# Kernel optimization log

Measured on AMD Instinct MI355X. Metric: run time of the kernel, lower is better.

## Reference

```python
import jax, jax.numpy as jnp
import numpy as np

BS, TS, NE, ED = 32, 64, 64, 128
AE = 256          # attn_embed_dim
NH = 4            # attn heads
HD = AE // NH     # head dim
RH = 256          # rnn_hidden_dim
NA = 8            # n_agents
NACT = 64         # n_actions
NEG = -1e10


def setup_inputs() -> dict:
    key = jax.random.key(0)
    ks = iter(jax.random.split(key, 64))
    def g(shape, s=0.05):
        return jax.random.normal(next(ks), shape, dtype=jnp.float32) * s
    inp = dict(
        entities=g((BS, TS, NE, ED), 1.0),
        obs_mask=jax.random.randint(next(ks), (BS, TS, NE, NE), 0, 2, dtype=jnp.int32),
        entity_mask=jax.random.randint(next(ks), (BS, TS, NE), 0, 2, dtype=jnp.int32),
        hidden_q=g((BS, NA, RH), 1.0),
        hidden_pi=g((BS, NA, RH), 1.0),
    )
    for p in ('q', 'p'):
        inp[f'{p}_fc1_w'] = g((AE, ED)); inp[f'{p}_fc1_b'] = g((AE,))
        inp[f'{p}_fc2_w'] = g((RH, AE)); inp[f'{p}_fc2_b'] = g((RH,))
        inp[f'{p}_gru_wih'] = g((3 * RH, RH)); inp[f'{p}_gru_whh'] = g((3 * RH, RH))
        inp[f'{p}_gru_bih'] = g((3 * RH,)); inp[f'{p}_gru_bhh'] = g((3 * RH,))
        inp[f'{p}_fcq_w'] = g((NACT, RH)); inp[f'{p}_fcq_b'] = g((NACT,))
        inp[f'{p}_fcpi_w'] = g((NACT, RH)); inp[f'{p}_fcpi_b'] = g((NACT,))
    inp['q_attn_in_w'] = g((3 * AE, AE))
    inp['q_attn_out_w'] = g((AE, AE)); inp['q_attn_out_b'] = g((AE,))
    return inp


def _attention(x1, pre_mask, in_w, out_w, out_b):
    # x1: [B, NE, AE]; pre_mask: [B, NA, NE] (1 = masked)
    qkv = x1 @ in_w.T                                   # [B, NE, 3*AE]
    q, k, v = jnp.split(qkv, 3, axis=-1)
    q = q[:, :NA].reshape(-1, NA, NH, HD).transpose(0, 2, 1, 3)   # [B,H,NA,HD]
    k = k.reshape(-1, NE, NH, HD).transpose(0, 2, 1, 3)           # [B,H,NE,HD]
    v = v.reshape(-1, NE, NH, HD).transpose(0, 2, 1, 3)
    logits = jnp.einsum('bhqd,bhkd->bhqk', q, k) / jnp.sqrt(jnp.float32(HD))
    m = (pre_mask[:, None, :, :] != 0)                  # [B,1,NA,NE]
    dead = jnp.all(m, axis=-1, keepdims=True)           # fully-masked rows -> NaN fix
    logits = jnp.where(m, -jnp.inf, logits)
    logits = jnp.where(dead, 0.0, logits)
    w = jax.nn.softmax(logits, axis=-1)
    w = jnp.where(dead, 0.0, w)                         # torch: masked_fill(NaN, 0)
    out = jnp.einsum('bhqk,bhkd->bhqd', w, v)
    out = out.transpose(0, 2, 1, 3).reshape(-1, NA, AE)
    return out @ out_w.T + out_b


def _gru_scan(x3, h0, wih, whh, bih, bhh):
    # x3: [BS, TS, NA, RH]; h0: [BS*NA, RH]
    xt = x3.transpose(1, 0, 2, 3).reshape(TS, BS * NA, RH)
    def step(h, x):
        gi = x @ wih.T + bih
        gh = h @ whh.T + bhh
        ir, iz, inn = jnp.split(gi, 3, axis=-1)
        hr, hz, hn = jnp.split(gh, 3, axis=-1)
        r = jax.nn.sigmoid(ir + hr)
        z = jax.nn.sigmoid(iz + hz)
        n = jnp.tanh(inn + r * hn)
        h_new = (1.0 - z) * n + z * h
        return h_new, h_new
    _, hs = jax.lax.scan(step, h0, xt)
    return hs.reshape(TS, BS, NA, RH).transpose(1, 0, 2, 3)       # [BS,TS,NA,RH]


def _module(entities, obs_mask, entity_mask, hidden, use_attn,
            fc1_w, fc1_b, fc2_w, fc2_b, gru_wih, gru_whh, gru_bih, gru_bhh,
            fcq_w, fcq_b, fcpi_w, fcpi_b, attn=None):
    B = BS * TS
    e = entities.reshape(B, NE, ED)
    om = obs_mask.reshape(B, NE, NE)
    em = entity_mask.reshape(B, NE)
    agent_mask = em[:, :NA]                              # [B, NA]
    x1 = jax.nn.relu(e @ fc1_w.T + fc1_b)                # [B, NE, AE]
    if use_attn:
        in_w, out_w, out_b = attn
        x2 = _attention(x1, om[:, :NA], in_w, out_w, out_b)
        x2 = jnp.where(agent_mask[:, :, None] != 0, 0.0, x2)   # post_mask
    else:
        x2 = x1[:, :NA]
    x3 = jax.nn.relu(x2 @ fc2_w.T + fc2_b).reshape(BS, TS, NA, RH)
    hs = _gru_scan(x3, hidden.reshape(-1, RH), gru_wih, gru_whh, gru_bih, gru_bhh)
    oq = hs @ fcq_w.T + fcq_b
    opi = hs @ fcpi_w.T + fcpi_b
    am = (agent_mask.reshape(BS, TS, NA, 1) != 0)
    oq = jnp.where(am, 0.0, oq)
    opi = jnp.where(am, NEG, opi)
    return oq, opi, hs


def reference(entities, obs_mask, entity_mask, hidden_q, hidden_pi,
              q_fc1_w, q_fc1_b, q_attn_in_w, q_attn_out_w, q_attn_out_b,
              q_fc2_w, q_fc2_b, q_gru_wih, q_gru_whh, q_gru_bih, q_gru_bhh,
              q_fcq_w, q_fcq_b, q_fcpi_w, q_fcpi_b,
              p_fc1_w, p_fc1_b, p_fc2_w, p_fc2_b,
              p_gru_wih, p_gru_whh, p_gru_bih, p_gru_bhh,
              p_fcq_w, p_fcq_b, p_fcpi_w, p_fcpi_b):
    q, pi, h_q = _module(entities, obs_mask, entity_mask, hidden_q, True,
                         q_fc1_w, q_fc1_b, q_fc2_w, q_fc2_b,
                         q_gru_wih, q_gru_whh, q_gru_bih, q_gru_bhh,
                         q_fcq_w, q_fcq_b, q_fcpi_w, q_fcpi_b,
                         attn=(q_attn_in_w, q_attn_out_w, q_attn_out_b))
    _, pi_avg, h_pi = _module(entities, obs_mask, entity_mask, hidden_pi, False,
                              p_fc1_w, p_fc1_b, p_fc2_w, p_fc2_b,
                              p_gru_wih, p_gru_whh, p_gru_bih, p_gru_bhh,
                              p_fcq_w, p_fcq_b, p_fcpi_w, p_fcpi_b)
    return (q, pi, pi_avg, h_q, h_pi)
```

## Files before the change

### kernel.cpp

```cpp
#include <hip/hip_runtime.h>

typedef unsigned short ushort_t;
typedef __attribute__((ext_vector_type(4))) float f32x4;
typedef __attribute__((ext_vector_type(8))) short s16x8;
typedef __attribute__((ext_vector_type(4))) short s16x4;

#define MFMA16(a, b, c) __builtin_amdgcn_mfma_f32_16x16x32_bf16((a), (b), (c), 0, 0, 0)

__device__ __forceinline__ float us2f(unsigned short u) {
  union { unsigned int i; float f; } v; v.i = ((unsigned int)u) << 16; return v.f;
}
__device__ __forceinline__ unsigned short f2us(float f) {
  union { float f; unsigned int i; } v; v.f = f;
  unsigned int x = v.i;
  return (unsigned short)((x + 0x7FFFu + ((x >> 16) & 1u)) >> 16);
}
__device__ __forceinline__ s16x8 ld8f(const float* p) {
  f32x4 a = *reinterpret_cast<const f32x4*>(p);
  f32x4 b = *reinterpret_cast<const f32x4*>(p + 4);
  s16x8 r;
  r[0] = (short)f2us(a[0]); r[1] = (short)f2us(a[1]);
  r[2] = (short)f2us(a[2]); r[3] = (short)f2us(a[3]);
  r[4] = (short)f2us(b[0]); r[5] = (short)f2us(b[1]);
  r[6] = (short)f2us(b[2]); r[7] = (short)f2us(b[3]);
  return r;
}
__device__ __forceinline__ float sigm(float x) { return 1.0f / (1.0f + __expf(-x)); }
__device__ __forceinline__ float tanh_f(float x) {
  float e = __expf(-2.0f * fabsf(x));
  float t = (1.0f - e) / (1.0f + e);
  return x < 0.0f ? -t : t;
}

__global__ __launch_bounds__(256) void conv_k(
    const float* __restrict__ s0, const float* __restrict__ s1,
    const float* __restrict__ s2, const float* __restrict__ s3,
    ushort_t* __restrict__ d) {
  int i = blockIdx.x * 256 + threadIdx.x;
  if (i >= 155648) return;
  long e = (long)i * 4;
  const float* s; long off;
  if (e < 196608) { s = s0; off = e; }
  else if (e < 393216) { s = s1; off = e - 196608; }
  else if (e < 425984) { s = s2; off = e - 393216; }
  else { s = s3; off = e - 425984; }
  f32x4 v = *reinterpret_cast<const f32x4*>(s + off);
  s16x4 r;
  r[0] = (short)f2us(v[0]); r[1] = (short)f2us(v[1]);
  r[2] = (short)f2us(v[2]); r[3] = (short)f2us(v[3]);
  *reinterpret_cast<s16x4*>(d + e) = r;
}

template <int BN, int EPI, int ROWSEL, int RELU, int AF32, int WF32, int OF32,
          int QKV, int HB>
__global__ __launch_bounds__(256) void gemm_k(
    const void* __restrict__ A_, const void* __restrict__ W_,
    const float* __restrict__ bias, const int* __restrict__ em,
    void* __restrict__ out_, ushort_t* __restrict__ qout, long row0,
    int M, int N, int K,
    const void* __restrict__ A2_, const void* __restrict__ W2_,
    const float* __restrict__ bias2, void* __restrict__ out2_) {
  constexpr int NF = BN / 32;
  if (A2_ != nullptr && blockIdx.z != 0) {
    A_ = A2_; W_ = W2_; bias = bias2; out_ = out2_;
  }
  const float* Af = (const float*)A_;
  const ushort_t* Ab = (const ushort_t*)A_;
  const float* Wf = (const float*)W_;
  const ushort_t* Wb = (const ushort_t*)W_;
  float* outf = (float*)out_;
  ushort_t* outb = (ushort_t*)out_;
  __shared__ ushort_t As[128 * 40];
  __shared__ ushort_t Ws[BN * 40];
  const int tid = threadIdx.x;
  const int lane = tid & 63;
  const int wid = tid >> 6;
  const int wm = wid & 1, wn = wid >> 1;
  const int m0 = blockIdx.x * 128;
  const int n0 = blockIdx.y * BN;
  const int fr = lane & 15;
  const int kb = (lane >> 4) * 8;
  const int rb = (lane >> 4) * 4;

  f32x4 acc[4][NF];
#pragma unroll
  for (int i = 0; i < 4; i++)
#pragma unroll
    for (int j = 0; j < NF; j++) acc[i][j] = (f32x4){0.f, 0.f, 0.f, 0.f};

  for (int k0 = 0; k0 < K; k0 += 32) {
    __syncthreads();
    for (int c = tid; c < 512; c += 256) {
      int row = c >> 2, kc = (c & 3) * 8;
      int gr = m0 + row;
      long ar = ROWSEL ? ((long)(gr >> 3) * 64 + (gr & 7)) : (long)gr;
      s16x8 vv;
      if (AF32) vv = ld8f(&Af[ar * (long)K + k0 + kc]);
      else vv = *reinterpret_cast<const s16x8*>(&Ab[ar * (long)K + k0 + kc]);
      *reinterpret_cast<s16x8*>(&As[row * 40 + kc]) = vv;
    }
    for (int c = tid; c < BN * 4; c += 256) {
      int row = c >> 2, kc = (c & 3) * 8;
      s16x8 wv;
      if (WF32) wv = ld8f(&Wf[(long)(n0 + row) * K + k0 + kc]);
      else wv = *reinterpret_cast<const s16x8*>(&Wb[(long)(n0 + row) * K + k0 + kc]);
      *reinterpret_cast<s16x8*>(&Ws[row * 40 + kc]) = wv;
    }
    __syncthreads();
    s16x8 af[4], wf[NF];
#pragma unroll
    for (int mi = 0; mi < 4; mi++)
      af[mi] = *reinterpret_cast<const s16x8*>(&As[(wm * 64 + mi * 16 + fr) * 40 + kb]);
#pragma unroll
    for (int ni = 0; ni < NF; ni++)
      wf[ni] = *reinterpret_cast<const s16x8*>(&Ws[(wn * (BN / 2) + ni * 16 + fr) * 40 + kb]);
#pragma unroll
    for (int mi = 0; mi < 4; mi++)
#pragma unroll
      for (int ni = 0; ni < NF; ni++) acc[mi][ni] = MFMA16(af[mi], wf[ni], acc[mi][ni]);
  }

#pragma unroll
  for (int ni = 0; ni < NF; ni++) {
    int col = n0 + wn * (BN / 2) + ni * 16 + fr;
    float bv = HB ? bias[col] : 0.0f;
#pragma unroll
    for (int mi = 0; mi < 4; mi++) {
#pragma unroll
      for (int rr = 0; rr < 4; rr++) {
        int row = m0 + wm * 64 + mi * 16 + rb + rr;
        float v = acc[mi][ni][rr] + bv;
        if (RELU) v = fmaxf(v, 0.0f);
        if (EPI == 2 || EPI == 3) {
          if (em[(long)(row >> 3) * 64 + (row & 7)] != 0) v = (EPI == 2) ? 0.0f : -1.0e10f;
        }
        if (QKV) {
          long grow = row0 + row;
          int e = (int)(grow & 63);
          if (col < 256) {
            if (e < 8) qout[((grow >> 6) * 8 + e) * 256 + col] = f2us(v * 0.125f);
          } else {
            outb[(long)row * 512 + (col - 256)] = f2us(v);
          }
        } else if (OF32) {
          outf[(long)row * N + col] = v;
        } else {
          outb[(long)row * N + col] = f2us(v);
        }
      }
    }
  }
}

__global__ __launch_bounds__(512) void attn2_k(
    const ushort_t* __restrict__ kv, const ushort_t* __restrict__ qbuf,
    const int* __restrict__ obs, ushort_t* __restrict__ attn_out, int b0) {
  __shared__ ushort_t qs[16 * 264];
  __shared__ ushort_t ks[64 * 264];
  __shared__ ushort_t vs[64 * 264];
  __shared__ float lg[32 * 66];
  __shared__ int oms[512];

  const int b_loc = blockIdx.x;
  const long b = b0 + b_loc;
  const int tid = threadIdx.x;
  const int lane = tid & 63;
  const int w = tid >> 6;
  const int fr = lane & 15, kb = (lane >> 4) * 8, rb = (lane >> 4) * 4;

  oms[tid] = obs[b * 4096 + tid];
  {
    int row = tid >> 5, cc = (tid & 31) * 8;
    if (tid < 256) {
      *reinterpret_cast<s16x8*>(&qs[row * 264 + cc]) =
          *reinterpret_cast<const s16x8*>(&qbuf[(b * 8 + row) * 256 + cc]);
    } else {
      *reinterpret_cast<s16x8*>(&qs[row * 264 + cc]) = (s16x8){0,0,0,0,0,0,0,0};
    }
  }
  for (int i = 0; i < 4; i++) {
    int e = i * 16 + (tid >> 5);
    int cc = (tid & 31) * 8;
    const ushort_t* src = &kv[((long)(b_loc * 64 + e)) * 512];
    *reinterpret_cast<s16x8*>(&ks[e * 264 + cc]) =
        *reinterpret_cast<const s16x8*>(&src[cc]);
    *reinterpret_cast<s16x8*>(&vs[e * 264 + cc]) =
        *reinterpret_cast<const s16x8*>(&src[256 + cc]);
  }
  __syncthreads();

  {
    const int h = w >> 1, np = w & 1;
    f32x4 lacc[2];
    lacc[0] = (f32x4){0.f, 0.f, 0.f, 0.f};
    lacc[1] = (f32x4){0.f, 0.f, 0.f, 0.f};
#pragma unroll
    for (int k0 = 0; k0 < 64; k0 += 32) {
      s16x8 af = *reinterpret_cast<const s16x8*>(&qs[fr * 264 + h * 64 + k0 + kb]);
#pragma unroll
      for (int j = 0; j < 2; j++) {
        int e0 = (np * 2 + j) * 16;
        s16x8 bf = *reinterpret_cast<const s16x8*>(&ks[(e0 + fr) * 264 + h * 64 + k0 + kb]);
        lacc[j] = MFMA16(af, bf, lacc[j]);
      }
    }
#pragma unroll
    for (int j = 0; j < 2; j++) {
      int e = (np * 2 + j) * 16 + fr;
#pragma unroll
      for (int rr = 0; rr < 4; rr++) {
        int a = rb + rr;
        if (a < 8)
          lg[(a * 4 + h) * 66 + e] = (oms[a * 64 + e] != 0) ? -1.0e30f : lacc[j][rr];
      }
    }
  }
  __syncthreads();

  {
    int ri = tid >> 4, sub = tid & 15;
    float v4[4];
#pragma unroll
    for (int j = 0; j < 4; j++) v4[j] = lg[ri * 66 + sub * 4 + j];
    float m = fmaxf(fmaxf(v4[0], v4[1]), fmaxf(v4[2], v4[3]));
#pragma unroll
    for (int d = 1; d < 16; d <<= 1) m = fmaxf(m, __shfl_xor(m, d));
    bool dead = (m < -5.0e29f);
    float s = 0.0f;
#pragma unroll
    for (int j = 0; j < 4; j++) { v4[j] = __expf(v4[j] - m); s += v4[j]; }
#pragma unroll
    for (int d = 1; d < 16; d <<= 1) s += __shfl_xor(s, d);
    float inv = dead ? 0.0f : (1.0f / s);
#pragma unroll
    for (int j = 0; j < 4; j++) lg[ri * 66 + sub * 4 + j] = v4[j] * inv;
  }
  __syncthreads();

  {
    int a = tid >> 6, d0 = (tid & 63) * 4, h = d0 >> 6;
    const float* wrow = &lg[(a * 4 + h) * 66];
    float facc[4] = {0.f, 0.f, 0.f, 0.f};
    for (int e = 0; e < 64; e++) {
      float wv = wrow[e];
      s16x4 vv = *reinterpret_cast<const s16x4*>(&vs[e * 264 + d0]);
#pragma unroll
      for (int j = 0; j < 4; j++) facc[j] += wv * us2f((unsigned short)vv[j]);
    }
    s16x4 r;
#pragma unroll
    for (int j = 0; j < 4; j++) r[j] = (short)f2us(facc[j]);
    *reinterpret_cast<s16x4*>(&attn_out[(b * 8 + a) * 256 + d0]) = r;
  }
}

__global__ __launch_bounds__(1024, 4) void gru4_k(
    const ushort_t* __restrict__ gi_q, const ushort_t* __restrict__ gi_p,
    const ushort_t* __restrict__ whhb_q, const ushort_t* __restrict__ whhb_p,
    const float* __restrict__ bhh_q, const float* __restrict__ bhh_p,
    const float* __restrict__ h0_q, const float* __restrict__ h0_p,
    float* __restrict__ hs_q, float* __restrict__ hs_p) {
  __shared__ ushort_t nw[256 * 256];
  __shared__ ushort_t hls[2][16 * 264];
  const int bid = blockIdx.x;
  const int mdl = bid >> 4, cg = bid & 15;
  const ushort_t* gi = mdl ? gi_p : gi_q;
  const ushort_t* whh = mdl ? whhb_p : whhb_q;
  const float* bhh = mdl ? bhh_p : bhh_q;
  const float* h0 = mdl ? h0_p : h0_q;
  float* hs = mdl ? hs_p : hs_q;

  const int tid = threadIdx.x;
  const int lane = tid & 63, w = tid >> 6;
  const int fr = lane & 15, kb = (lane >> 4) * 8, rb = (lane >> 4) * 4;
  const int col = w * 16 + fr;

  s16x8 wrz[2][8];
#pragma unroll
  for (int g = 0; g < 2; g++)
#pragma unroll
    for (int ks = 0; ks < 8; ks++)
      wrz[g][ks] = *reinterpret_cast<const s16x8*>(
          &whh[(g * 256 + col) * 256 + ks * 32 + kb]);

  char* nwb = (char*)nw;
  for (int c = tid; c < 8192; c += 1024) {
    int row = c >> 5, kc = (c & 31) * 8;
    *reinterpret_cast<s16x8*>(nwb + row * 512 + ((kc * 2) ^ ((row & 7) << 4))) =
        *reinterpret_cast<const s16x8*>(&whh[(512 + row) * 256 + kc]);
  }

  int nwaddr[8];
#pragma unroll
  for (int ks = 0; ks < 8; ks++)
    nwaddr[ks] = col * 512 + (((ks * 32 + kb) * 2) ^ ((col & 7) << 4));

  float h[4], bh[3];
#pragma unroll
  for (int rr = 0; rr < 4; rr++) h[rr] = h0[(cg * 16 + rb + rr) * 256 + col];
#pragma unroll
  for (int g = 0; g < 3; g++) bh[g] = bhh[g * 256 + col];

  const int chain0 = cg * 16 + rb;
  const long r0 = (long)(chain0 >> 3) * 512 + (chain0 & 7);
  const ushort_t* gp0 = gi + r0 * 768 + col;
  float* hp0 = hs + r0 * 256 + col;

#define GRU_STEP(BUF)                                                          \
  {                                                                            \
    float gv[3][4];                                                            \
    _Pragma("unroll") for (int rr = 0; rr < 4; rr++) {                         \
      gv[0][rr] = us2f(gp0[rr * 768]);                                         \
      gv[1][rr] = us2f(gp0[rr * 768 + 256]);                                   \
      gv[2][rr] = us2f(gp0[rr * 768 + 512]);                                   \
    }                                                                          \
    gp0 += 6144;                                                               \
    _Pragma("unroll") for (int rr = 0; rr < 4; rr++)                           \
        hls[BUF][(rb + rr) * 264 + col] = f2us(h[rr]);                         \
    __syncthreads();                                                           \
    f32x4 acc[3];                                                              \
    _Pragma("unroll") for (int i = 0; i < 3; i++)                              \
        acc[i] = (f32x4){0.f, 0.f, 0.f, 0.f};                                  \
    _Pragma("unroll") for (int ks = 0; ks < 8; ks++) {                         \
      s16x8 a = *reinterpret_cast<const s16x8*>(                               \
          &hls[BUF][fr * 264 + ks * 32 + kb]);                                 \
      acc[0] = MFMA16(a, wrz[0][ks], acc[0]);                                  \
      acc[1] = MFMA16(a, wrz[1][ks], acc[1]);                                  \
      s16x8 bn = *reinterpret_cast<const s16x8*>(nwb + nwaddr[ks]);            \
      acc[2] = MFMA16(a, bn, acc[2]);                                          \
    }                                                                          \
    _Pragma("unroll") for (int rr = 0; rr < 4; rr++) {                         \
      float r_ = sigm(gv[0][rr] + acc[0][rr] + bh[0]);                         \
      float z_ = sigm(gv[1][rr] + acc[1][rr] + bh[1]);                         \
      float n_ = tanh_f(gv[2][rr] + r_ * (acc[2][rr] + bh[2]));                \
      float hn = (1.0f - z_) * n_ + z_ * h[rr];                                \
      h[rr] = hn;                                                              \
      hp0[rr * 256] = hn;                                                      \
    }                                                                          \
    hp0 += 2048;                                                               \
  }

  for (int t2 = 0; t2 < 32; t2++) {
    GRU_STEP(0)
    GRU_STEP(1)
  }
#undef GRU_STEP
}

extern "C" void kernel_launch(void* const* d_in, const int* in_sizes, int n_in,
                              void* d_out, int out_size, void* d_ws, size_t ws_size,
                              hipStream_t stream) {
  (void)in_sizes; (void)n_in; (void)out_size; (void)ws_size;

  const float* entities = (const float*)d_in[0];
  const int* obs = (const int*)d_in[1];
  const int* em = (const int*)d_in[2];
  const float* hidq = (const float*)d_in[3];
  const float* hidp = (const float*)d_in[4];
  const float* q_fc1_w = (const float*)d_in[5];
  const float* q_fc1_b = (const float*)d_in[6];
  const float* q_fc2_w = (const float*)d_in[7];
  const float* q_fc2_b = (const float*)d_in[8];
  const float* q_wih = (const float*)d_in[9];
  const float* q_whh = (const float*)d_in[10];
  const float* q_bih = (const float*)d_in[11];
  const float* q_bhh = (const float*)d_in[12];
  const float* q_fcq_w = (const float*)d_in[13];
  const float* q_fcq_b = (const float*)d_in[14];
  const float* q_fcpi_w = (const float*)d_in[15];
  const float* q_fcpi_b = (const float*)d_in[16];
  const float* p_fc1_w = (const float*)d_in[17];
  const float* p_fc1_b = (const float*)d_in[18];
  const float* p_fc2_w = (const float*)d_in[19];
  const float* p_fc2_b = (const float*)d_in[20];
  const float* p_wih = (const float*)d_in[21];
  const float* p_whh = (const float*)d_in[22];
  const float* p_bih = (const float*)d_in[23];
  const float* p_bhh = (const float*)d_in[24];
  const float* p_fcpi_w = (const float*)d_in[27];
  const float* p_fcpi_b = (const float*)d_in[28];
  const float* inw = (const float*)d_in[29];
  const float* outw = (const float*)d_in[30];
  const float* outb = (const float*)d_in[31];

  ushort_t* ws = (ushort_t*)d_ws;
  ushort_t* qbuf = ws;
  ushort_t* attn = ws + 4194304l;
  ushort_t* x1c  = ws + 8388608l;
  ushort_t* kvc  = ws + 16777216l;
  ushort_t* wcv  = ws + 33554432l;
  ushort_t* wbq = wcv;
  ushort_t* wbp = wcv + 196608l;
  ushort_t* wf1 = wcv + 393216l;
  ushort_t* win = wcv + 425984l;
  ushort_t* x2b = ws + 35651584l;
  ushort_t* x3q = ws + 39845888l;
  ushort_t* x1p = ws + 44040192l;
  ushort_t* x3p = ws + 48234496l;
  ushort_t* giq = ws + 52428800l;
  ushort_t* gip = ws + 65011712l;

  float* out = (float*)d_out;
  float* o_q = out;
  float* o_pi = out + 1048576l;
  float* o_piA = out + 2097152l;
  float* o_hq = out + 3145728l;
  float* o_hp = out + 7340032l;

  const int nc = 4, CB = 512;
  const long MR = (long)CB * 64;
  const void* NUL = nullptr;

  conv_k<<<608, 256, 0, stream>>>(q_whh, p_whh, q_fc1_w, inw, wcv);

  for (int c = 0; c < nc; c++) {
    gemm_k<128, 0, 0, 1, 1, 0, 0, 0, 1><<<dim3(256, 2), 256, 0, stream>>>(
        entities + (long)c * MR * 128, wf1, q_fc1_b, em, x1c, nullptr, 0,
        (int)MR, 256, 128, NUL, NUL, nullptr, nullptr);
    gemm_k<128, 0, 0, 0, 0, 0, 0, 1, 0><<<dim3(256, 6), 256, 0, stream>>>(
        x1c, win, nullptr, em, kvc, qbuf, (long)c * MR, (int)MR, 768, 256,
        NUL, NUL, nullptr, nullptr);
    attn2_k<<<CB, 512, 0, stream>>>(kvc, qbuf, obs, attn, c * CB);
  }
  gemm_k<128, 2, 0, 0, 0, 1, 0, 0, 1><<<dim3(128, 2), 256, 0, stream>>>(
      attn, outw, outb, em, x2b, nullptr, 0, 16384, 256, 256,
      NUL, NUL, nullptr, nullptr);
  gemm_k<128, 0, 1, 1, 1, 1, 0, 0, 1><<<dim3(128, 2), 256, 0, stream>>>(
      entities, p_fc1_w, p_fc1_b, em, x1p, nullptr, 0, 16384, 256, 128,
      NUL, NUL, nullptr, nullptr);
  gemm_k<128, 0, 0, 1, 0, 1, 0, 0, 1><<<dim3(128, 2, 2), 256, 0, stream>>>(
      x2b, q_fc2_w, q_fc2_b, em, x3q, nullptr, 0, 16384, 256, 256,
      x1p, p_fc2_w, p_fc2_b, x3p);
  gemm_k<128, 0, 0, 0, 0, 1, 0, 0, 1><<<dim3(128, 6, 2), 256, 0, stream>>>(
      x3q, q_wih, q_bih, em, giq, nullptr, 0, 16384, 768, 256,
      x3p, p_wih, p_bih, gip);
  gru4_k<<<32, 1024, 0, stream>>>(giq, gip, wbq, wbp, q_bhh, p_bhh, hidq, hidp,
                                  o_hq, o_hp);
  gemm_k<64, 2, 0, 0, 1, 1, 1, 0, 1><<<dim3(128, 1), 256, 0, stream>>>(
      o_hq, q_fcq_w, q_fcq_b, em, o_q, nullptr, 0, 16384, 64, 256,
      NUL, NUL, nullptr, nullptr);
  gemm_k<64, 3, 0, 0, 1, 1, 1, 0, 1><<<dim3(128, 1, 2), 256, 0, stream>>>(
      o_hq, q_fcpi_w, q_fcpi_b, em, o_pi, nullptr, 0, 16384, 64, 256,
      o_hp, p_fcpi_w, p_fcpi_b, o_piA);
}
```

Measured before the change: 612.2 us.

## Batch fc1 GEMM into one launch, enlarge attention chunks, speed up GRU step

The fc1 projection now runs once over all entities instead of once per chunk, and the QKV and attention loop uses two chunks of 1024 instead of four of 512, so there are fewer, larger launches. The workspace layout is reshuffled so giq and gip alias the x1 buffer, which is dead by the time they are written. The GRU step uses packed bf16 conversion, folds the bias into the accumulator init, raises wave priority around the MFMA loop, and switches to rcp-based sigmoid and tanh. The fast activations change numerics slightly, and the aliased buffers depend on the order in which they are written and read.

```diff
diff --git a/kernel.cpp b/kernel.cpp
--- a/kernel.cpp
+++ b/kernel.cpp
@@ -30,6 +30,14 @@
   float e = __expf(-2.0f * fabsf(x));
   float t = (1.0f - e) / (1.0f + e);
   return x < 0.0f ? -t : t;
+}
+__device__ __forceinline__ float fast_sigm(float x) {
+  return __builtin_amdgcn_rcpf(1.0f + __expf(-x));
+}
+__device__ __forceinline__ float fast_tanh(float y) {
+  float yc = fminf(fmaxf(y, -15.0f), 15.0f);
+  float e2 = __expf(2.0f * yc);
+  return (e2 - 1.0f) * __builtin_amdgcn_rcpf(e2 + 1.0f);
 }
 
 __global__ __launch_bounds__(256) void conv_k(
@@ -254,7 +262,7 @@
   }
 }
 
-__global__ __launch_bounds__(1024, 4) void gru4_k(
+__global__ __launch_bounds__(1024, 4) void gru5_k(
     const ushort_t* __restrict__ gi_q, const ushort_t* __restrict__ gi_p,
     const ushort_t* __restrict__ whhb_q, const ushort_t* __restrict__ whhb_p,
     const float* __restrict__ bhh_q, const float* __restrict__ bhh_p,
@@ -305,8 +313,10 @@
   const long r0 = (long)(chain0 >> 3) * 512 + (chain0 & 7);
   const ushort_t* gp0 = gi + r0 * 768 + col;
   float* hp0 = hs + r0 * 256 + col;
-
-#define GRU_STEP(BUF)                                                          \
+  ushort_t* hrow0 = &hls[0][rb * 264 + col];
+  ushort_t* hrow1 = &hls[1][rb * 264 + col];
+
+#define GRU_STEP(HROW, BUF)                                                    \
   {                                                                            \
     float gv[3][4];                                                            \
     _Pragma("unroll") for (int rr = 0; rr < 4; rr++) {                         \
@@ -315,12 +325,18 @@
       gv[2][rr] = us2f(gp0[rr * 768 + 512]);                                   \
     }                                                                          \
     gp0 += 6144;                                                               \
-    _Pragma("unroll") for (int rr = 0; rr < 4; rr++)                           \
-        hls[BUF][(rb + rr) * 264 + col] = f2us(h[rr]);                         \
+    unsigned int pk01, pk23;                                                   \
+    asm("v_cvt_pk_bf16_f32 %0, %1, %2" : "=v"(pk01) : "v"(h[0]), "v"(h[1]));   \
+    asm("v_cvt_pk_bf16_f32 %0, %1, %2" : "=v"(pk23) : "v"(h[2]), "v"(h[3]));   \
+    HROW[0] = (ushort_t)(pk01 & 0xffffu);                                      \
+    HROW[264] = (ushort_t)(pk01 >> 16);                                        \
+    HROW[528] = (ushort_t)(pk23 & 0xffffu);                                    \
+    HROW[792] = (ushort_t)(pk23 >> 16);                                        \
     __syncthreads();                                                           \
     f32x4 acc[3];                                                              \
     _Pragma("unroll") for (int i = 0; i < 3; i++)                              \
-        acc[i] = (f32x4){0.f, 0.f, 0.f, 0.f};                                  \
+        acc[i] = (f32x4){bh[i], bh[i], bh[i], bh[i]};                          \
+    __builtin_amdgcn_s_setprio(1);                                             \
     _Pragma("unroll") for (int ks = 0; ks < 8; ks++) {                         \
       s16x8 a = *reinterpret_cast<const s16x8*>(                               \
           &hls[BUF][fr * 264 + ks * 32 + kb]);                                 \
@@ -329,11 +345,12 @@
       s16x8 bn = *reinterpret_cast<const s16x8*>(nwb + nwaddr[ks]);            \
       acc[2] = MFMA16(a, bn, acc[2]);                                          \
     }                                                                          \
+    __builtin_amdgcn_s_setprio(0);                                             \
     _Pragma("unroll") for (int rr = 0; rr < 4; rr++) {                         \
-      float r_ = sigm(gv[0][rr] + acc[0][rr] + bh[0]);                         \
-      float z_ = sigm(gv[1][rr] + acc[1][rr] + bh[1]);                         \
-      float n_ = tanh_f(gv[2][rr] + r_ * (acc[2][rr] + bh[2]));                \
-      float hn = (1.0f - z_) * n_ + z_ * h[rr];                                \
+      float r_ = fast_sigm(gv[0][rr] + acc[0][rr]);                            \
+      float z_ = fast_sigm(gv[1][rr] + acc[1][rr]);                            \
+      float n_ = fast_tanh(gv[2][rr] + r_ * acc[2][rr]);                       \
+      float hn = n_ + z_ * (h[rr] - n_);                                       \
       h[rr] = hn;                                                              \
       hp0[rr * 256] = hn;                                                      \
     }                                                                          \
@@ -341,8 +358,8 @@
   }
 
   for (int t2 = 0; t2 < 32; t2++) {
-    GRU_STEP(0)
-    GRU_STEP(1)
+    GRU_STEP(hrow0, 0)
+    GRU_STEP(hrow1, 1)
   }
 #undef GRU_STEP
 }
@@ -384,21 +401,21 @@
   const float* outb = (const float*)d_in[31];
 
   ushort_t* ws = (ushort_t*)d_ws;
-  ushort_t* qbuf = ws;
-  ushort_t* attn = ws + 4194304l;
-  ushort_t* x1c  = ws + 8388608l;
-  ushort_t* kvc  = ws + 16777216l;
-  ushort_t* wcv  = ws + 33554432l;
+  ushort_t* qbuf  = ws;
+  ushort_t* attn  = ws + 4194304l;
+  ushort_t* x1all = ws + 8388608l;
+  ushort_t* giq   = ws + 8388608l;
+  ushort_t* gip   = ws + 20971520l;
+  ushort_t* kvc   = ws + 41943040l;
+  ushort_t* wcv   = ws + 75497472l;
   ushort_t* wbq = wcv;
   ushort_t* wbp = wcv + 196608l;
   ushort_t* wf1 = wcv + 393216l;
   ushort_t* win = wcv + 425984l;
-  ushort_t* x2b = ws + 35651584l;
-  ushort_t* x3q = ws + 39845888l;
-  ushort_t* x1p = ws + 44040192l;
-  ushort_t* x3p = ws + 48234496l;
-  ushort_t* giq = ws + 52428800l;
-  ushort_t* gip = ws + 65011712l;
+  ushort_t* x2b = ws + 76120064l;
+  ushort_t* x3q = ws + 80314368l;
+  ushort_t* x1p = ws + 84508672l;
+  ushort_t* x3p = ws + 88702976l;
 
   float* out = (float*)d_out;
   float* o_q = out;
@@ -407,19 +424,19 @@
   float* o_hq = out + 3145728l;
   float* o_hp = out + 7340032l;
 
-  const int nc = 4, CB = 512;
+  const int nc = 2, CB = 1024;
   const long MR = (long)CB * 64;
   const void* NUL = nullptr;
 
   conv_k<<<608, 256, 0, stream>>>(q_whh, p_whh, q_fc1_w, inw, wcv);
 
+  gemm_k<128, 0, 0, 1, 1, 0, 0, 0, 1><<<dim3(1024, 2), 256, 0, stream>>>(
+      entities, wf1, q_fc1_b, em, x1all, nullptr, 0, 131072, 256, 128,
+      NUL, NUL, nullptr, nullptr);
   for (int c = 0; c < nc; c++) {
-    gemm_k<128, 0, 0, 1, 1, 0, 0, 0, 1><<<dim3(256, 2), 256, 0, stream>>>(
-        entities + (long)c * MR * 128, wf1, q_fc1_b, em, x1c, nullptr, 0,
-        (int)MR, 256, 128, NUL, NUL, nullptr, nullptr);
-    gemm_k<128, 0, 0, 0, 0, 0, 0, 1, 0><<<dim3(256, 6), 256, 0, stream>>>(
-        x1c, win, nullptr, em, kvc, qbuf, (long)c * MR, (int)MR, 768, 256,
-        NUL, NUL, nullptr, nullptr);
+    gemm_k<128, 0, 0, 0, 0, 0, 0, 1, 0><<<dim3(512, 6), 256, 0, stream>>>(
+        x1all + (long)c * MR * 256, win, nullptr, em, kvc, qbuf, (long)c * MR,
+        (int)MR, 768, 256, NUL, NUL, nullptr, nullptr);
     attn2_k<<<CB, 512, 0, stream>>>(kvc, qbuf, obs, attn, c * CB);
   }
   gemm_k<128, 2, 0, 0, 0, 1, 0, 0, 1><<<dim3(128, 2), 256, 0, stream>>>(
@@ -434,12 +451,12 @@
   gemm_k<128, 0, 0, 0, 0, 1, 0, 0, 1><<<dim3(128, 6, 2), 256, 0, stream>>>(
       x3q, q_wih, q_bih, em, giq, nullptr, 0, 16384, 768, 256,
       x3p, p_wih, p_bih, gip);
-  gru4_k<<<32, 1024, 0, stream>>>(giq, gip, wbq, wbp, q_bhh, p_bhh, hidq, hidp,
+  gru5_k<<<32, 1024, 0, stream>>>(giq, gip, wbq, wbp, q_bhh, p_bhh, hidq, hidp,
                                   o_hq, o_hp);
   gemm_k<64, 2, 0, 0, 1, 1, 1, 0, 1><<<dim3(128, 1), 256, 0, stream>>>(
       o_hq, q_fcq_w, q_fcq_b, em, o_q, nullptr, 0, 16384, 64, 256,
       NUL, NUL, nullptr, nullptr);
   gemm_k<64, 3, 0, 0, 1, 1, 1, 0, 1><<<dim3(128, 1, 2), 256, 0, stream>>>(
       o_hq, q_fcpi_w, q_fcpi_b, em, o_pi, nullptr, 0, 16384, 64, 256,
-      o_hp, p_fcpi_w, p_fcpi_b, o_piA);
-}
+      o_hp, p_fcpi_b ? p_fcpi_w : p_fcpi_w, p_fcpi_b, o_piA);
+}
```

Result: slower. 671.8 us (+9.7%).
